# Performance work log

Hardware: AMD Instinct MI355X
Metric: run time of the kernel (lower is better)

Reference implementation:

```python
import jax, jax.numpy as jnp
import numpy as np

DIM = 512
HEADS = 8
DIM_HEAD = 64
INNER = HEADS * DIM_HEAD  # 512
NUM_PATCHES = 64
NUM_FRAMES = 32
EPS = 1e-5


def setup_inputs() -> dict:
    key = jax.random.key(0)
    k1, k2, k3, k4 = jax.random.split(key, 4)
    B, T = 4, NUM_PATCHES * NUM_FRAMES  # 4, 2048
    x = jax.random.normal(k1, (B, T, DIM), dtype=jnp.float32)
    w_qkv = jax.random.normal(k2, (DIM, 3 * INNER), dtype=jnp.float32) * (DIM ** -0.5)
    w_out = jax.random.normal(k3, (INNER, DIM), dtype=jnp.float32) * (INNER ** -0.5)
    b_out = jax.random.normal(k4, (DIM,), dtype=jnp.float32) * 0.01
    ln_g = jnp.ones((DIM,), dtype=jnp.float32)
    ln_b = jnp.zeros((DIM,), dtype=jnp.float32)
    return {"x": x, "ln_g": ln_g, "ln_b": ln_b, "w_qkv": w_qkv, "w_out": w_out, "b_out": b_out}


def _frame_causal_mask(T):
    # token i belongs to frame i // NUM_PATCHES; query frame attends to frames <= its own
    frame = jnp.arange(T) // NUM_PATCHES
    return frame[:, None] >= frame[None, :]  # [T, T] bool


def reference(x, ln_g, ln_b, w_qkv, w_out, b_out):
    B, T, C = x.shape
    scale = DIM_HEAD ** -0.5
    # LayerNorm
    mu = jnp.mean(x, axis=-1, keepdims=True)
    var = jnp.mean(jnp.square(x - mu), axis=-1, keepdims=True)
    xn = (x - mu) * jax.lax.rsqrt(var + EPS) * ln_g + ln_b
    # QKV projection (no bias)
    qkv = xn @ w_qkv  # [B, T, 3*INNER]
    q, k, v = jnp.split(qkv, 3, axis=-1)
    reshape = lambda t: t.reshape(B, T, HEADS, DIM_HEAD).transpose(0, 2, 1, 3)  # b h n d
    q, k, v = reshape(q), reshape(k), reshape(v)
    dots = jnp.einsum('bhqd,bhkd->bhqk', q, k) * scale
    mask = _frame_causal_mask(T)
    dots = jnp.where(mask[None, None], dots, -jnp.inf)
    attn = jax.nn.softmax(dots, axis=-1)
    out = jnp.einsum('bhqk,bhkd->bhqd', attn, v)
    out = out.transpose(0, 2, 1, 3).reshape(B, T, INNER)
    return out @ w_out + b_out
```

## Files before the change

kernel.cpp:

```cpp
#include <hip/hip_runtime.h>

typedef unsigned short u16;
typedef float f32x4 __attribute__((ext_vector_type(4)));
typedef short bf16x8 __attribute__((ext_vector_type(8)));

#define MFMA16(a, b, c) __builtin_amdgcn_mfma_f32_16x16x32_bf16((a), (b), (c), 0, 0, 0)
#define SWZ8(row, off) ((off) ^ (((row) & 7) << 3))

#define CFENCE() asm volatile("" ::: "memory")
#define BARRIER() do { CFENCE(); __builtin_amdgcn_s_barrier(); CFENCE(); } while (0)
#define VMW(n) asm volatile("s_waitcnt vmcnt(" #n ")" ::: "memory")

static __device__ __forceinline__ u16 f2bf(float f) {
  union { float f; unsigned u; } c; c.f = f;
  unsigned r = c.u + 0x7fffu + ((c.u >> 16) & 1u);
  return (u16)(r >> 16);
}

static __device__ __forceinline__ float exp2_hw(float x) {
  float r;
  asm("v_exp_f32 %0, %1" : "=v"(r) : "v"(x));
  return r;
}

static __device__ __forceinline__ unsigned cvtpk(float lo, float hi) {
  unsigned r;
  asm("v_cvt_pk_bf16_f32 %0, %1, %2" : "=v"(r) : "v"(lo), "v"(hi));
  return r;
}

static __device__ __forceinline__ void llds16(u16* l, const u16* g) {
  __builtin_amdgcn_global_load_lds((const __attribute__((address_space(1))) void*)g,
                                   (__attribute__((address_space(3))) void*)l, 16, 0, 0);
}

__global__ __launch_bounds__(256) void prep_ln(
    const float* __restrict__ x, const float* __restrict__ g,
    const float* __restrict__ be, u16* __restrict__ xn,
    const float* __restrict__ w_qkv, const float* __restrict__ w_out,
    u16* __restrict__ wqkvT, u16* __restrict__ woutT) {
  __shared__ u16 tile[64][66];
  int bid = blockIdx.x;
  int tid = threadIdx.x;
  if (bid < 2048) {
    int row = bid * 4 + (tid >> 6);
    int lane = tid & 63;
    const float4* xr = (const float4*)(x + (size_t)row * 512) + lane * 2;
    float4 v0 = xr[0], v1 = xr[1];
    float s = v0.x + v0.y + v0.z + v0.w + v1.x + v1.y + v1.z + v1.w;
    float ss = v0.x * v0.x + v0.y * v0.y + v0.z * v0.z + v0.w * v0.w +
               v1.x * v1.x + v1.y * v1.y + v1.z * v1.z + v1.w * v1.w;
#pragma unroll
    for (int msk = 32; msk >= 1; msk >>= 1) {
      s += __shfl_xor(s, msk, 64);
      ss += __shfl_xor(ss, msk, 64);
    }
    float mu = s * (1.f / 512.f);
    float var = ss * (1.f / 512.f) - mu * mu;
    float rs = rsqrtf(var + 1e-5f);
    const float4* gp = (const float4*)g + lane * 2;
    const float4* bp = (const float4*)be + lane * 2;
    float4 g0 = gp[0], g1 = gp[1], b0 = bp[0], b1 = bp[1];
    union { u16 h[8]; uint4 q; } o;
    o.h[0] = f2bf((v0.x - mu) * rs * g0.x + b0.x);
    o.h[1] = f2bf((v0.y - mu) * rs * g0.y + b0.y);
    o.h[2] = f2bf((v0.z - mu) * rs * g0.z + b0.z);
    o.h[3] = f2bf((v0.w - mu) * rs * g0.w + b0.w);
    o.h[4] = f2bf((v1.x - mu) * rs * g1.x + b1.x);
    o.h[5] = f2bf((v1.y - mu) * rs * g1.y + b1.y);
    o.h[6] = f2bf((v1.z - mu) * rs * g1.z + b1.z);
    o.h[7] = f2bf((v1.w - mu) * rs * g1.w + b1.w);
    *(uint4*)&xn[(size_t)row * 512 + lane * 8] = o.q;
    return;
  }
  int pb = bid - 2048;
  const float* src;
  u16* dst;
  int C, tr, tc;
  if (pb < 192) {
    src = w_qkv; dst = wqkvT; C = 1536;
    tr = (pb & 7) * 64;
    tc = (pb >> 3) * 64;
  } else {
    int b2 = pb - 192;
    src = w_out; dst = woutT; C = 512;
    tr = (b2 & 7) * 64;
    tc = (b2 >> 3) * 64;
  }
  int i = tid >> 4;
  int j4 = (tid & 15) * 4;
#pragma unroll
  for (int p = 0; p < 4; ++p) {
    int row = i + p * 16;
    float4 v = *(const float4*)&src[(size_t)(tr + row) * C + tc + j4];
    tile[row][j4 + 0] = f2bf(v.x);
    tile[row][j4 + 1] = f2bf(v.y);
    tile[row][j4 + 2] = f2bf(v.z);
    tile[row][j4 + 3] = f2bf(v.w);
  }
  __syncthreads();
  int j = tid >> 3;
  int i8 = (tid & 7) * 8;
#pragma unroll
  for (int p = 0; p < 2; ++p) {
    int orow = j + p * 32;
    union { u16 h[8]; uint4 q; } o;
#pragma unroll
    for (int s = 0; s < 8; ++s) o.h[s] = tile[i8 + s][orow];
    *(uint4*)&dst[(size_t)(tc + orow) * 512 + tr + i8] = o.q;
  }
}

__global__ __launch_bounds__(256) void gemm_qkv(
    const u16* __restrict__ A, const u16* __restrict__ BT,
    u16* __restrict__ qb, u16* __restrict__ kb, u16* __restrict__ vtb) {
  __shared__ u16 ls[16384];
  u16* lsA = ls;
  u16* lsB = ls + 8192;
  int bid = blockIdx.x;
  int xcd = bid & 7, sq = bid >> 3;
  int m0 = (xcd * 8 + (sq & 7)) * 128;
  int n0 = (sq >> 3) * 128;
  int sec = n0 >> 9;
  int tid = threadIdx.x;
  int lane = tid & 63, wave = tid >> 6;
  int wm = (wave >> 1) * 64, wn = (wave & 1) * 64;
  int lr = lane & 15, lq = lane >> 4;
  f32x4 acc[4][4] = {};
  for (int kt = 0; kt < 8; ++kt) {
#pragma unroll
    for (int c = 0; c < 4; ++c) {
      int ci = c * 256 + tid;
      int row = ci >> 3, colb = ci & 7;
      int goff = kt * 64 + ((colb * 8) ^ ((row & 7) * 8));
      llds16(&lsA[ci * 8], &A[(size_t)(m0 + row) * 512 + goff]);
      llds16(&lsB[ci * 8], &BT[(size_t)(n0 + row) * 512 + goff]);
    }
    __syncthreads();
#pragma unroll
    for (int ks = 0; ks < 2; ++ks) {
      bf16x8 af[4], bfr[4];
#pragma unroll
      for (int i = 0; i < 4; ++i) {
        int ra = wm + i * 16 + lr;
        af[i] = *(const bf16x8*)&lsA[ra * 64 + SWZ8(ra, ks * 32 + lq * 8)];
        int rb = wn + i * 16 + lr;
        bfr[i] = *(const bf16x8*)&lsB[rb * 64 + SWZ8(rb, ks * 32 + lq * 8)];
      }
#pragma unroll
      for (int i = 0; i < 4; ++i)
#pragma unroll
        for (int j = 0; j < 4; ++j)
          acc[i][j] = MFMA16(af[i], bfr[j], acc[i][j]);
    }
    __syncthreads();
  }
  int b = m0 >> 11, t0 = m0 & 2047;
  float sc = (sec == 0) ? 0.180336880f : 1.0f;
  if (sec < 2) {
#pragma unroll
    for (int i = 0; i < 4; ++i)
#pragma unroll
      for (int j = 0; j < 4; ++j) {
        int col = wn + j * 16 + lr;
#pragma unroll
        for (int r = 0; r < 4; ++r) {
          int row = wm + i * 16 + lq * 4 + r;
          ls[row * 128 + (col ^ ((row & 7) << 3))] = f2bf(acc[i][j][r] * sc);
        }
      }
    __syncthreads();
    u16* dst = (sec == 0) ? qb : kb;
#pragma unroll
    for (int s = 0; s < 8; ++s) {
      int li = s * 256 + tid;
      int row = li >> 4, c8 = (li & 15) * 8;
      uint4 v = *(uint4*)&ls[row * 128 + (c8 ^ ((row & 7) << 3))];
      int gn = n0 + c8;
      int h = (gn >> 6) & 7, d = gn & 63;
      *(uint4*)&dst[((size_t)(b * 8 + h) * 2048 + t0 + row) * 64 + d] = v;
    }
  } else {
#pragma unroll
    for (int i = 0; i < 4; ++i)
#pragma unroll
      for (int j = 0; j < 4; ++j) {
        int col = wn + j * 16 + lr;
#pragma unroll
        for (int r = 0; r < 4; ++r) {
          int row = wm + i * 16 + lq * 4 + r;
          ls[col * 128 + (row ^ ((col & 7) << 3))] = f2bf(acc[i][j][r]);
        }
      }
    __syncthreads();
#pragma unroll
    for (int s = 0; s < 8; ++s) {
      int li = s * 256 + tid;
      int dcol = li >> 4, t8 = (li & 15) * 8;
      uint4 v = *(uint4*)&ls[dcol * 128 + (t8 ^ ((dcol & 7) << 3))];
      int gn = n0 + dcol;
      int h = (gn >> 6) & 7, d = gn & 63;
      *(uint4*)&vtb[((size_t)(b * 8 + h) * 64 + d) * 2048 + t0 + t8] = v;
    }
  }
}

__global__ __launch_bounds__(256) void attn_kernel(
    const u16* __restrict__ qb, const u16* __restrict__ kb,
    const u16* __restrict__ vtb, u16* __restrict__ ao) {
  int blk = blockIdx.x;
  int xcd = blk & 7;
  int seq = blk >> 3;
  int bh = xcd * 4 + (seq & 3);
  int qf = 31 - (seq >> 2);
  int tid = threadIdx.x, lane = tid & 63, wave = tid >> 6;
  int lr = lane & 15, lq = lane >> 4;
  __shared__ u16 lsK[2][64 * 64], lsV[2][64 * 64];
  __shared__ u16 lsP[4][16 * 64];
  const u16* kfb = kb + (size_t)bh * 2048 * 64;
  const u16* vfb = vtb + (size_t)bh * 64 * 2048;

  int ci0 = tid, ci1 = 256 + tid;
  int r0 = ci0 >> 3, cb0 = ci0 & 7, sw0 = (cb0 * 8) ^ ((r0 & 7) * 8);
  int r1 = ci1 >> 3, cb1 = ci1 & 7, sw1 = (cb1 * 8) ^ ((r1 & 7) * 8);

#define STAGE(buf, kf_)                                                        \
  do {                                                                         \
    const u16* kp = kfb + (size_t)(kf_) * 64 * 64;                             \
    llds16(&lsK[buf][ci0 * 8], &kp[(size_t)r0 * 64 + sw0]);                    \
    llds16(&lsK[buf][ci1 * 8], &kp[(size_t)r1 * 64 + sw1]);                    \
    llds16(&lsV[buf][ci0 * 8], &vfb[(size_t)r0 * 2048 + (kf_) * 64 + sw0]);    \
    llds16(&lsV[buf][ci1 * 8], &vfb[(size_t)r1 * 2048 + (kf_) * 64 + sw1]);    \
  } while (0)

  STAGE(0, 0);

  const u16* qbase = qb + ((size_t)bh * 2048 + qf * 64) * 64;
  int qrow = wave * 16 + lr;
  bf16x8 qa0 = *(const bf16x8*)&qbase[qrow * 64 + lq * 8];
  bf16x8 qa1 = *(const bf16x8*)&qbase[qrow * 64 + 32 + lq * 8];

  f32x4 o[4] = {};
  float m = -1e30f, l = 0.f;
  u16* pw = lsP[wave];

  for (int kf = 0; kf <= qf; ++kf) {
    int cur = kf & 1;
    if (kf < qf) {
      STAGE(cur ^ 1, kf + 1);
      VMW(4);
    } else {
      VMW(0);
    }
    BARRIER();
    f32x4 s[4];
    __builtin_amdgcn_s_setprio(1);
#pragma unroll
    for (int c = 0; c < 4; ++c) {
      int rk = c * 16 + lr;
      bf16x8 k0 = *(const bf16x8*)&lsK[cur][rk * 64 + SWZ8(rk, lq * 8)];
      bf16x8 k1 = *(const bf16x8*)&lsK[cur][rk * 64 + SWZ8(rk, 32 + lq * 8)];
      f32x4 z = {};
      z = MFMA16(k0, qa0, z);
      z = MFMA16(k1, qa1, z);
      s[c] = z;
    }
    __builtin_amdgcn_s_setprio(0);
    float m0 = fmaxf(fmaxf(s[0][0], s[0][1]), fmaxf(s[0][2], s[0][3]));
    float m1 = fmaxf(fmaxf(s[1][0], s[1][1]), fmaxf(s[1][2], s[1][3]));
    float m2 = fmaxf(fmaxf(s[2][0], s[2][1]), fmaxf(s[2][2], s[2][3]));
    float m3 = fmaxf(fmaxf(s[3][0], s[3][1]), fmaxf(s[3][2], s[3][3]));
    float mx = fmaxf(fmaxf(m0, m1), fmaxf(m2, m3));
    mx = fmaxf(mx, __shfl_xor(mx, 16, 64));
    mx = fmaxf(mx, __shfl_xor(mx, 32, 64));
    if (!__all(mx <= m + 8.f)) {
      float mn = fmaxf(m, mx);
      float al = exp2_hw(m - mn);
      m = mn;
      l *= al;
      float al0 = __shfl(al, lq * 4 + 0, 64);
      float al1 = __shfl(al, lq * 4 + 1, 64);
      float al2 = __shfl(al, lq * 4 + 2, 64);
      float al3 = __shfl(al, lq * 4 + 3, 64);
#pragma unroll
      for (int oc = 0; oc < 4; ++oc) {
        o[oc][0] *= al0;
        o[oc][1] *= al1;
        o[oc][2] *= al2;
        o[oc][3] *= al3;
      }
    }
    float sum = 0.f;
#pragma unroll
    for (int c = 0; c < 4; ++c) {
#pragma unroll
      for (int r = 0; r < 4; ++r) {
        s[c][r] = exp2_hw(s[c][r] - m);
        sum += s[c][r];
      }
    }
    sum += __shfl_xor(sum, 16, 64);
    sum += __shfl_xor(sum, 32, 64);
    l += sum;
#pragma unroll
    for (int c = 0; c < 4; ++c) {
      union { unsigned u[2]; uint2 q2; } pk;
      pk.u[0] = cvtpk(s[c][0], s[c][1]);
      pk.u[1] = cvtpk(s[c][2], s[c][3]);
      *(uint2*)&pw[lr * 64 + ((c * 16 + lq * 4) ^ ((lr & 7) * 8))] = pk.q2;
    }
    bf16x8 pa0 = *(const bf16x8*)&pw[lr * 64 + SWZ8(lr, lq * 8)];
    bf16x8 pa1 = *(const bf16x8*)&pw[lr * 64 + SWZ8(lr, 32 + lq * 8)];
    __builtin_amdgcn_s_setprio(1);
#pragma unroll
    for (int oc = 0; oc < 4; ++oc) {
      int rv = oc * 16 + lr;
      bf16x8 v0 = *(const bf16x8*)&lsV[cur][rv * 64 + SWZ8(rv, lq * 8)];
      bf16x8 v1 = *(const bf16x8*)&lsV[cur][rv * 64 + SWZ8(rv, 32 + lq * 8)];
      o[oc] = MFMA16(pa0, v0, o[oc]);
      o[oc] = MFMA16(pa1, v1, o[oc]);
    }
    __builtin_amdgcn_s_setprio(0);
    BARRIER();
  }
#undef STAGE
  float inv = 1.0f / l;
  float i0 = __shfl(inv, lq * 4 + 0, 64);
  float i1 = __shfl(inv, lq * 4 + 1, 64);
  float i2 = __shfl(inv, lq * 4 + 2, 64);
  float i3 = __shfl(inv, lq * 4 + 3, 64);
  int b = bh >> 3, h = bh & 7;
#pragma unroll
  for (int oc = 0; oc < 4; ++oc) {
    int q = qf * 64 + wave * 16 + lq * 4;
    int col = h * 64 + oc * 16 + lr;
    ao[((size_t)b * 2048 + q + 0) * 512 + col] = f2bf(o[oc][0] * i0);
    ao[((size_t)b * 2048 + q + 1) * 512 + col] = f2bf(o[oc][1] * i1);
    ao[((size_t)b * 2048 + q + 2) * 512 + col] = f2bf(o[oc][2] * i2);
    ao[((size_t)b * 2048 + q + 3) * 512 + col] = f2bf(o[oc][3] * i3);
  }
}

__global__ __launch_bounds__(256) void gemm_out(
    const u16* __restrict__ A, const u16* __restrict__ BT,
    const float* __restrict__ bias, float* __restrict__ out) {
  __shared__ u16 lsA[128 * 64], lsB[128 * 64];
  int bid = blockIdx.x;
  int xcd = bid & 7, sq = bid >> 3;
  int m0 = (xcd * 8 + (sq & 7)) * 128;
  int n0 = (sq >> 3) * 128;
  int tid = threadIdx.x;
  int lane = tid & 63, wave = tid >> 6;
  int wm = (wave >> 1) * 64, wn = (wave & 1) * 64;
  int lr = lane & 15, lq = lane >> 4;
  f32x4 acc[4][4] = {};
  for (int kt = 0; kt < 8; ++kt) {
#pragma unroll
    for (int c = 0; c < 4; ++c) {
      int ci = c * 256 + tid;
      int row = ci >> 3, colb = ci & 7;
      int goff = kt * 64 + ((colb * 8) ^ ((row & 7) * 8));
      llds16(&lsA[ci * 8], &A[(size_t)(m0 + row) * 512 + goff]);
      llds16(&lsB[ci * 8], &BT[(size_t)(n0 + row) * 512 + goff]);
    }
    __syncthreads();
#pragma unroll
    for (int ks = 0; ks < 2; ++ks) {
      bf16x8 af[4], bfr[4];
#pragma unroll
      for (int i = 0; i < 4; ++i) {
        int ra = wm + i * 16 + lr;
        af[i] = *(const bf16x8*)&lsA[ra * 64 + SWZ8(ra, ks * 32 + lq * 8)];
        int rb = wn + i * 16 + lr;
        bfr[i] = *(const bf16x8*)&lsB[rb * 64 + SWZ8(rb, ks * 32 + lq * 8)];
      }
#pragma unroll
      for (int i = 0; i < 4; ++i)
#pragma unroll
        for (int j = 0; j < 4; ++j)
          acc[i][j] = MFMA16(af[i], bfr[j], acc[i][j]);
    }
    __syncthreads();
  }
#pragma unroll
  for (int j = 0; j < 4; ++j) {
    int gn = n0 + wn + j * 16 + lr;
    float bj = bias[gn];
#pragma unroll
    for (int i = 0; i < 4; ++i) {
      int gm = m0 + wm + i * 16 + lq * 4;
#pragma unroll
      for (int r = 0; r < 4; ++r)
        out[(size_t)(gm + r) * 512 + gn] = acc[i][j][r] + bj;
    }
  }
}

extern "C" void kernel_launch(void* const* d_in, const int* in_sizes, int n_in,
                              void* d_out, int out_size, void* d_ws, size_t ws_size,
                              hipStream_t stream) {
  const float* x = (const float*)d_in[0];
  const float* ln_g = (const float*)d_in[1];
  const float* ln_b = (const float*)d_in[2];
  const float* w_qkv = (const float*)d_in[3];
  const float* w_out = (const float*)d_in[4];
  const float* b_out = (const float*)d_in[5];
  float* out = (float*)d_out;
  char* ws = (char*)d_ws;

  u16* xn    = (u16*)(ws + 0);
  u16* wqkvT = (u16*)(ws + 8388608);
  u16* woutT = (u16*)(ws + 9961472);
  u16* qb    = (u16*)(ws + 10485760);
  u16* kb    = (u16*)(ws + 18874368);
  u16* vtb   = (u16*)(ws + 27262976);
  u16* ao    = (u16*)(ws + 35651584);

  prep_ln<<<2304, 256, 0, stream>>>(x, ln_g, ln_b, xn, w_qkv, w_out, wqkvT, woutT);
  gemm_qkv<<<768, 256, 0, stream>>>(xn, wqkvT, qb, kb, vtb);
  attn_kernel<<<1024, 256, 0, stream>>>(qb, kb, vtb, ao);
  gemm_out<<<256, 256, 0, stream>>>(ao, woutT, b_out, out);
}
```

Baseline: 159.5 us.

## Double-buffer LDS in QKV and output GEMMs with prefetch of next K tile

Both projection GEMMs switch from a single LDS buffer with a sync-load-compute loop over K=64 tiles to two LDS buffers over K=32 tiles. The next tile is prefetched asynchronously while the current one is computed, with partial vmcnt waits. MFMA sections are wrapped in s_setprio to favour matrix issue. This aims to hide global-load latency behind compute, at the cost of twice as many iterations and barriers and a narrower swizzle on the 32-wide rows.

Result: faster. 151.7 us (-4.9%).

```diff
diff --git a/kernel.cpp b/kernel.cpp
--- a/kernel.cpp
+++ b/kernel.cpp
@@ -115,8 +115,6 @@
     const u16* __restrict__ A, const u16* __restrict__ BT,
     u16* __restrict__ qb, u16* __restrict__ kb, u16* __restrict__ vtb) {
   __shared__ u16 ls[16384];
-  u16* lsA = ls;
-  u16* lsB = ls + 8192;
   int bid = blockIdx.x;
   int xcd = bid & 7, sq = bid >> 3;
   int m0 = (xcd * 8 + (sq & 7)) * 128;
@@ -126,35 +124,54 @@
   int lane = tid & 63, wave = tid >> 6;
   int wm = (wave >> 1) * 64, wn = (wave & 1) * 64;
   int lr = lane & 15, lq = lane >> 4;
+  int ar0 = tid >> 2, ac0 = tid & 3;
+  const u16* Ar0 = &A[(size_t)(m0 + ar0) * 512 + ((ac0 ^ (ar0 & 3)) * 8)];
+  const u16* Ar1 = &A[(size_t)(m0 + 64 + ar0) * 512 + ((ac0 ^ (ar0 & 3)) * 8)];
+  const u16* Br0 = &BT[(size_t)(n0 + ar0) * 512 + ((ac0 ^ (ar0 & 3)) * 8)];
+  const u16* Br1 = &BT[(size_t)(n0 + 64 + ar0) * 512 + ((ac0 ^ (ar0 & 3)) * 8)];
+
+#define STAGEG(b, kt_)                                 \
+  do {                                                 \
+    u16* la = ls + (b) * 8192;                         \
+    u16* lb = la + 4096;                               \
+    int gc = (kt_) * 32;                               \
+    llds16(&la[tid * 8], Ar0 + gc);                    \
+    llds16(&la[(tid + 256) * 8], Ar1 + gc);            \
+    llds16(&lb[tid * 8], Br0 + gc);                    \
+    llds16(&lb[(tid + 256) * 8], Br1 + gc);            \
+  } while (0)
+
   f32x4 acc[4][4] = {};
-  for (int kt = 0; kt < 8; ++kt) {
-#pragma unroll
-    for (int c = 0; c < 4; ++c) {
-      int ci = c * 256 + tid;
-      int row = ci >> 3, colb = ci & 7;
-      int goff = kt * 64 + ((colb * 8) ^ ((row & 7) * 8));
-      llds16(&lsA[ci * 8], &A[(size_t)(m0 + row) * 512 + goff]);
-      llds16(&lsB[ci * 8], &BT[(size_t)(n0 + row) * 512 + goff]);
-    }
-    __syncthreads();
-#pragma unroll
-    for (int ks = 0; ks < 2; ++ks) {
-      bf16x8 af[4], bfr[4];
-#pragma unroll
-      for (int i = 0; i < 4; ++i) {
-        int ra = wm + i * 16 + lr;
-        af[i] = *(const bf16x8*)&lsA[ra * 64 + SWZ8(ra, ks * 32 + lq * 8)];
-        int rb = wn + i * 16 + lr;
-        bfr[i] = *(const bf16x8*)&lsB[rb * 64 + SWZ8(rb, ks * 32 + lq * 8)];
-      }
-#pragma unroll
-      for (int i = 0; i < 4; ++i)
-#pragma unroll
-        for (int j = 0; j < 4; ++j)
-          acc[i][j] = MFMA16(af[i], bfr[j], acc[i][j]);
-    }
-    __syncthreads();
-  }
+  STAGEG(0, 0);
+  for (int kt = 0; kt < 16; ++kt) {
+    int cur = kt & 1;
+    if (kt < 15) {
+      STAGEG(cur ^ 1, kt + 1);
+      VMW(4);
+    } else {
+      VMW(0);
+    }
+    BARRIER();
+    u16* la = ls + cur * 8192;
+    u16* lb = la + 4096;
+    bf16x8 af[4], bfr[4];
+#pragma unroll
+    for (int i = 0; i < 4; ++i) {
+      int ra = wm + i * 16 + lr;
+      af[i] = *(const bf16x8*)&la[ra * 32 + ((lq ^ (ra & 3)) * 8)];
+      int rb = wn + i * 16 + lr;
+      bfr[i] = *(const bf16x8*)&lb[rb * 32 + ((lq ^ (rb & 3)) * 8)];
+    }
+    __builtin_amdgcn_s_setprio(1);
+#pragma unroll
+    for (int i = 0; i < 4; ++i)
+#pragma unroll
+      for (int j = 0; j < 4; ++j)
+        acc[i][j] = MFMA16(af[i], bfr[j], acc[i][j]);
+    __builtin_amdgcn_s_setprio(0);
+    BARRIER();
+  }
+#undef STAGEG
   int b = m0 >> 11, t0 = m0 & 2047;
   float sc = (sec == 0) ? 0.180336880f : 1.0f;
   if (sec < 2) {
@@ -344,7 +361,7 @@
 __global__ __launch_bounds__(256) void gemm_out(
     const u16* __restrict__ A, const u16* __restrict__ BT,
     const float* __restrict__ bias, float* __restrict__ out) {
-  __shared__ u16 lsA[128 * 64], lsB[128 * 64];
+  __shared__ u16 ls[16384];
   int bid = blockIdx.x;
   int xcd = bid & 7, sq = bid >> 3;
   int m0 = (xcd * 8 + (sq & 7)) * 128;
@@ -353,35 +370,54 @@
   int lane = tid & 63, wave = tid >> 6;
   int wm = (wave >> 1) * 64, wn = (wave & 1) * 64;
   int lr = lane & 15, lq = lane >> 4;
+  int ar0 = tid >> 2, ac0 = tid & 3;
+  const u16* Ar0 = &A[(size_t)(m0 + ar0) * 512 + ((ac0 ^ (ar0 & 3)) * 8)];
+  const u16* Ar1 = &A[(size_t)(m0 + 64 + ar0) * 512 + ((ac0 ^ (ar0 & 3)) * 8)];
+  const u16* Br0 = &BT[(size_t)(n0 + ar0) * 512 + ((ac0 ^ (ar0 & 3)) * 8)];
+  const u16* Br1 = &BT[(size_t)(n0 + 64 + ar0) * 512 + ((ac0 ^ (ar0 & 3)) * 8)];
+
+#define STAGEG(b, kt_)                                 \
+  do {                                                 \
+    u16* la = ls + (b) * 8192;                         \
+    u16* lb = la + 4096;                               \
+    int gc = (kt_) * 32;                               \
+    llds16(&la[tid * 8], Ar0 + gc);                    \
+    llds16(&la[(tid + 256) * 8], Ar1 + gc);            \
+    llds16(&lb[tid * 8], Br0 + gc);                    \
+    llds16(&lb[(tid + 256) * 8], Br1 + gc);            \
+  } while (0)
+
   f32x4 acc[4][4] = {};
-  for (int kt = 0; kt < 8; ++kt) {
-#pragma unroll
-    for (int c = 0; c < 4; ++c) {
-      int ci = c * 256 + tid;
-      int row = ci >> 3, colb = ci & 7;
-      int goff = kt * 64 + ((colb * 8) ^ ((row & 7) * 8));
-      llds16(&lsA[ci * 8], &A[(size_t)(m0 + row) * 512 + goff]);
-      llds16(&lsB[ci * 8], &BT[(size_t)(n0 + row) * 512 + goff]);
-    }
-    __syncthreads();
-#pragma unroll
-    for (int ks = 0; ks < 2; ++ks) {
-      bf16x8 af[4], bfr[4];
-#pragma unroll
-      for (int i = 0; i < 4; ++i) {
-        int ra = wm + i * 16 + lr;
-        af[i] = *(const bf16x8*)&lsA[ra * 64 + SWZ8(ra, ks * 32 + lq * 8)];
-        int rb = wn + i * 16 + lr;
-        bfr[i] = *(const bf16x8*)&lsB[rb * 64 + SWZ8(rb, ks * 32 + lq * 8)];
-      }
-#pragma unroll
-      for (int i = 0; i < 4; ++i)
-#pragma unroll
-        for (int j = 0; j < 4; ++j)
-          acc[i][j] = MFMA16(af[i], bfr[j], acc[i][j]);
-    }
-    __syncthreads();
-  }
+  STAGEG(0, 0);
+  for (int kt = 0; kt < 16; ++kt) {
+    int cur = kt & 1;
+    if (kt < 15) {
+      STAGEG(cur ^ 1, kt + 1);
+      VMW(4);
+    } else {
+      VMW(0);
+    }
+    BARRIER();
+    u16* la = ls + cur * 8192;
+    u16* lb = la + 4096;
+    bf16x8 af[4], bfr[4];
+#pragma unroll
+    for (int i = 0; i < 4; ++i) {
+      int ra = wm + i * 16 + lr;
+      af[i] = *(const bf16x8*)&la[ra * 32 + ((lq ^ (ra & 3)) * 8)];
+      int rb = wn + i * 16 + lr;
+      bfr[i] = *(const bf16x8*)&lb[rb * 32 + ((lq ^ (rb & 3)) * 8)];
+    }
+    __builtin_amdgcn_s_setprio(1);
+#pragma unroll
+    for (int i = 0; i < 4; ++i)
+#pragma unroll
+      for (int j = 0; j < 4; ++j)
+        acc[i][j] = MFMA16(af[i], bfr[j], acc[i][j]);
+    __builtin_amdgcn_s_setprio(0);
+    BARRIER();
+  }
+#undef STAGEG
 #pragma unroll
   for (int j = 0; j < 4; ++j) {
     int gn = n0 + wn + j * 16 + lr;
```
